# Kernel optimization log

Measured on AMD Instinct MI355X. Metric: run time of the kernel, lower is better.

The kernel has to match this reference:

```python
import jax, jax.numpy as jnp
import numpy as np
from jax import lax

_CLIP_MIN = 1e-06
_CLIP_MAX = 1.0
_POS_ALPHA = 0.0005
NUM_CLASSES = 21
RADIUS = 3
HALF_D = RADIUS * RADIUS
POOL = 3
PAD = POOL // 2
IGNORE = 255
LAM = 0.5  # loss_weight_lambda, lambda_way=1


def _max_pool(x):
    # NCHW max pool, kernel=stride=3, padding=1
    return lax.reduce_window(x, -jnp.inf, lax.max,
                             (1, 1, POOL, POOL), (1, 1, POOL, POOL),
                             ((0, 0), (0, 0), (PAD, PAD), (PAD, PAD)))


def _get_pairs(x):
    # stack radius*radius shifted crops -> [N, C, r^2, nh, nw]
    h, w = x.shape[2], x.shape[3]
    nh, nw = h - RADIUS + 1, w - RADIUS + 1
    crops = [x[:, :, y:y + nh, xo:xo + nw] for y in range(RADIUS) for xo in range(RADIUS)]
    return jnp.stack(crops, axis=2)


def _log_det_by_cholesky(m):
    chol = jnp.linalg.cholesky(m)
    return 2.0 * jnp.sum(jnp.log(jnp.diagonal(chol, axis1=-2, axis2=-1) + 1e-08), axis=-1)


def _rmi_lower_bound(labels_4d, probs_4d):
    la = _max_pool(labels_4d)
    pr = _max_pool(probs_4d)
    n, c = la.shape[0], la.shape[1]
    la_v = _get_pairs(la).reshape(n, c, HALF_D, -1)   # [N,C,d,L]
    pr_v = _get_pairs(pr).reshape(n, c, HALF_D, -1)
    la_v = la_v - jnp.mean(la_v, axis=3, keepdims=True)
    pr_v = pr_v - jnp.mean(pr_v, axis=3, keepdims=True)
    la_cov = jnp.einsum('ncdl,ncel->ncde', la_v, la_v)
    pr_cov = jnp.einsum('ncdl,ncel->ncde', pr_v, pr_v)
    eye = jnp.eye(HALF_D, dtype=la_cov.dtype)
    pr_cov_inv = jnp.linalg.inv(pr_cov + eye * _POS_ALPHA)
    la_pr_cov = jnp.einsum('ncdl,ncel->ncde', la_v, pr_v)
    appro_var = la_cov - jnp.einsum('ncde,ncef,ncgf->ncdg', la_pr_cov, pr_cov_inv, la_pr_cov)
    rmi_now = 0.5 * _log_det_by_cholesky(appro_var + eye * _POS_ALPHA)  # [N,C]
    rmi_per_class = jnp.mean(rmi_now.reshape(-1, NUM_CLASSES), axis=0) / float(HALF_D)
    return jnp.sum(rmi_per_class)


def setup_inputs() -> dict:
    key = jax.random.key(0)
    k1, k2 = jax.random.split(key)
    score = jax.random.normal(k1, (4, NUM_CLASSES, 512, 512), dtype=jnp.float32)
    target = jax.random.randint(k2, (4, 512, 512), 0, NUM_CLASSES, dtype=jnp.int64)
    return {"score": score, "target": target}


def reference(score, target):
    # cross entropy with ignore_index=255, mean reduction
    logp = jax.nn.log_softmax(score, axis=1)                      # [N,C,H,W]
    valid_ce = (target != IGNORE)
    safe_t = jnp.where(valid_ce, target, 0)
    nll = -jnp.take_along_axis(logp, safe_t[:, None].astype(jnp.int32), axis=1)[:, 0]
    normal_loss = jnp.sum(jnp.where(valid_ce, nll, 0.0)) / jnp.sum(valid_ce.astype(jnp.float32))

    # valid one-hot labels and masked sigmoid probs
    mask = (target < NUM_CLASSES)                                 # [N,H,W]
    maskf = mask.astype(jnp.float32)
    onehot = jax.nn.one_hot((target * mask).astype(jnp.int32), NUM_CLASSES, dtype=jnp.float32)
    onehot = onehot * maskf[..., None]                            # [N,H,W,C]
    onehot = jnp.transpose(onehot, (0, 3, 1, 2))                  # [N,C,H,W]
    probs = jnp.clip(jax.nn.sigmoid(score) * maskf[:, None], _CLIP_MIN, _CLIP_MAX)

    rmi_loss = _rmi_lower_bound(onehot, probs)
    return LAM * normal_loss + rmi_loss * (1.0 - LAM)
```

## Files before the change

kernel.cpp:

```cpp
#include <hip/hip_runtime.h>
#include <cfloat>
#include <cmath>

#define DEVINL __device__ __forceinline__

constexpr int N_ = 4, C_ = 21, H_ = 512, W_ = 512;
constexpr int P_ = 171;
constexpr int Q_ = 169;
constexpr int NC_ = N_ * C_;
constexpr int HW_ = H_ * W_;
constexpr int PP_ = P_ * P_;
constexpr int NCOV_ = 189;
constexpr float EPS_ = 5e-4f;
constexpr int RC_ = 29;
constexpr int G_ = 43;

DEVINL constexpr int tstart(int d) { return d * 9 - d * (d - 1) / 2; }

DEVINL float wave_sum(float v) {
#pragma unroll
    for (int o = 32; o > 0; o >>= 1) v += __shfl_down(v, o, 64);
    return v;
}

__global__ __launch_bounds__(256) void k_bits(const int* __restrict__ target,
                                              unsigned* __restrict__ pack) {
    int tid = blockIdx.x * 256 + threadIdx.x;
    if (tid >= N_ * PP_) return;
    int cell = tid % PP_;
    int n = tid / PP_;
    int j = cell % P_;
    int i = cell / P_;
    int hl = 3 * i - 1; if (hl < 0) hl = 0;
    int wl = 3 * j - 1; if (wl < 0) wl = 0;
    int hmax = 3 * i + 1, wmax = 3 * j + 1;
    const int* tb = target + (size_t)n * HW_;
    unsigned oh = 0, px = 0;
#pragma unroll
    for (int r = 0; r < 3; ++r) {
        int hh = hl + r;
        bool hv = hh <= hmax;
        const int* trow = tb + hh * W_;
#pragma unroll
        for (int dc = 0; dc < 3; ++dc) {
            int ww = wl + dc;
            int t = trow[ww];
            if (hv && (ww <= wmax) && t >= 0 && t < C_) {
                oh |= 1u << t;
                px |= 1u << (r * 3 + dc);
            }
        }
    }
    pack[tid] = oh | (px << 23);
}

__global__ __launch_bounds__(256) void k_ce(const float* __restrict__ score,
                                            const int* __restrict__ target,
                                            float* __restrict__ cov_ce) {
    int tid = blockIdx.x * 256 + threadIdx.x;
    int p0 = tid * 4;
    int n = p0 >> 18;
    int hw = p0 & (HW_ - 1);
    const float* sp = score + (size_t)n * C_ * HW_ + hw;

    float4 s[C_];
#pragma unroll
    for (int c = 0; c < C_; ++c)
        s[c] = *(const float4*)(sp + (size_t)c * HW_);
    int4 t4 = *(const int4*)(target + p0);

    float4 se = {0.f, 0.f, 0.f, 0.f};
    float4 stgt = {0.f, 0.f, 0.f, 0.f};
#pragma unroll
    for (int c = 0; c < C_; ++c) {
        se.x += __expf(s[c].x);
        se.y += __expf(s[c].y);
        se.z += __expf(s[c].z);
        se.w += __expf(s[c].w);
        if (t4.x == c) stgt.x = s[c].x;
        if (t4.y == c) stgt.y = s[c].y;
        if (t4.z == c) stgt.z = s[c].z;
        if (t4.w == c) stgt.w = s[c].w;
    }
    float nll = 0.f, cnt = 0.f;
    if (t4.x != 255) { nll += __logf(se.x) - stgt.x; cnt += 1.f; }
    if (t4.y != 255) { nll += __logf(se.y) - stgt.y; cnt += 1.f; }
    if (t4.z != 255) { nll += __logf(se.z) - stgt.z; cnt += 1.f; }
    if (t4.w != 255) { nll += __logf(se.w) - stgt.w; cnt += 1.f; }

    nll = wave_sum(nll);
    cnt = wave_sum(cnt);
    __shared__ float rn[4], rc[4];
    int wv = threadIdx.x >> 6, lane = threadIdx.x & 63;
    if (lane == 0) { rn[wv] = nll; rc[wv] = cnt; }
    __syncthreads();
    if (threadIdx.x == 0) {
        atomicAdd(&cov_ce[NC_ * NCOV_ + 0], rn[0] + rn[1] + rn[2] + rn[3]);
        atomicAdd(&cov_ce[NC_ * NCOV_ + 1], rc[0] + rc[1] + rc[2] + rc[3]);
    }
}

template <int IDX>
DEVINL void do_cell(const float (&f)[3][16], unsigned pk, int c, float* prp, float* lap) {
    unsigned px = pk >> 23;
    float vm = -FLT_MAX;
#pragma unroll
    for (int r = 0; r < 3; ++r)
#pragma unroll
        for (int dc = 0; dc < 3; ++dc)
            vm = fmaxf(vm, ((px >> (r * 3 + dc)) & 1u) ? f[r][IDX + dc] : -FLT_MAX);
    float p = __builtin_amdgcn_rcpf(1.f + __expf(-vm));
    p = fminf(fmaxf(p, 1e-6f), 1.f);
    *prp = p;
    *lap = ((pk >> c) & 1u) ? 1.f : 0.f;
}

__global__ __launch_bounds__(256) void k_pool(const float* __restrict__ score,
                                              const unsigned* __restrict__ pack,
                                              float* __restrict__ pr,
                                              float* __restrict__ la) {
    int tid = blockIdx.x * 256 + threadIdx.x;
    if (tid >= NC_ * P_ * G_) return;
    int g = tid % G_;
    int rest = tid / G_;
    int i = rest % P_;
    int ncidx = rest / P_;
    int n = ncidx / C_;
    int c = ncidx - n * C_;

    int hl = 3 * i - 1; if (hl < 0) hl = 0;
    int b = (g == 0) ? 0 : 12 * g - 4;
    int o3 = (b + 15 < W_) ? 12 : 8;

    const float* sb = score + (size_t)ncidx * HW_ + (size_t)hl * W_ + b;
    float f[3][16];
#pragma unroll
    for (int r = 0; r < 3; ++r) {
        const float* rp = sb + r * W_;
        float4 q0 = *(const float4*)(rp);
        float4 q1 = *(const float4*)(rp + 4);
        float4 q2 = *(const float4*)(rp + 8);
        float4 q3 = *(const float4*)(rp + o3);
        f[r][0] = q0.x;  f[r][1] = q0.y;  f[r][2] = q0.z;  f[r][3] = q0.w;
        f[r][4] = q1.x;  f[r][5] = q1.y;  f[r][6] = q1.z;  f[r][7] = q1.w;
        f[r][8] = q2.x;  f[r][9] = q2.y;  f[r][10] = q2.z; f[r][11] = q2.w;
        f[r][12] = q3.x; f[r][13] = q3.y; f[r][14] = q3.z; f[r][15] = q3.w;
    }

    const unsigned* pkp = pack + n * PP_ + i * P_ + 4 * g;
    size_t ob = (size_t)ncidx * PP_ + (size_t)i * P_ + 4 * g;
    if (g == 0) {
        do_cell<0>(f, pkp[0], c, pr + ob + 0, la + ob + 0);
        do_cell<2>(f, pkp[1], c, pr + ob + 1, la + ob + 1);
        do_cell<5>(f, pkp[2], c, pr + ob + 2, la + ob + 2);
        do_cell<8>(f, pkp[3], c, pr + ob + 3, la + ob + 3);
    } else {
        do_cell<3>(f, pkp[0], c, pr + ob + 0, la + ob + 0);
        do_cell<6>(f, pkp[1], c, pr + ob + 1, la + ob + 1);
        do_cell<9>(f, pkp[2], c, pr + ob + 2, la + ob + 2);
        if (4 * g + 3 < P_)
            do_cell<12>(f, pkp[3], c, pr + ob + 3, la + ob + 3);
    }
}

__global__ __launch_bounds__(256, 4) void k_cov(const float* __restrict__ la,
                                                const float* __restrict__ pr,
                                                float* __restrict__ cov) {
    int nc = blockIdx.x;
    int chunk = blockIdx.y;
    int part = blockIdx.z;
    int r0 = chunk * RC_;
    int rend = r0 + RC_;
    if (rend > Q_) rend = Q_;
    int npts = (rend - r0) * Q_;

    __shared__ float red[4][81];
    int lane = threadIdx.x & 63;
    int wv = threadIdx.x >> 6;

    if (part < 2) {
        const float* X = (part == 0 ? la : pr) + (size_t)nc * PP_;
        float s1[9], s2[45];
#pragma unroll
        for (int k = 0; k < 9; ++k) s1[k] = 0.f;
#pragma unroll
        for (int k = 0; k < 45; ++k) s2[k] = 0.f;
        for (int idx = threadIdx.x; idx < npts; idx += 256) {
            int lr = idx / Q_;
            int col = idx - lr * Q_;
            const float* xp = X + (r0 + lr) * P_ + col;
            float a[9];
#pragma unroll
            for (int dy = 0; dy < 3; ++dy)
#pragma unroll
                for (int dx = 0; dx < 3; ++dx) a[dy * 3 + dx] = xp[dy * P_ + dx];
#pragma unroll
            for (int d = 0; d < 9; ++d) s1[d] += a[d];
            int k = 0;
#pragma unroll
            for (int d = 0; d < 9; ++d)
#pragma unroll
                for (int e = d; e < 9; ++e) { s2[k] += a[d] * a[e]; ++k; }
        }
#pragma unroll
        for (int k = 0; k < 9; ++k) { float v = wave_sum(s1[k]); if (lane == 0) red[wv][k] = v; }
#pragma unroll
        for (int k = 0; k < 45; ++k) { float v = wave_sum(s2[k]); if (lane == 0) red[wv][9 + k] = v; }
        __syncthreads();
        int b1 = (part == 0) ? 0 : 9;
        int b2 = (part == 0) ? 18 : 63;
        for (int k = threadIdx.x; k < 54; k += 256) {
            float v = red[0][k] + red[1][k] + red[2][k] + red[3][k];
            int dst = (k < 9) ? (b1 + k) : (b2 + k - 9);
            atomicAdd(&cov[nc * NCOV_ + dst], v);
        }
    } else {
        const float* A = la + (size_t)nc * PP_;
        const float* B = pr + (size_t)nc * PP_;
        float sab[81];
#pragma unroll
        for (int k = 0; k < 81; ++k) sab[k] = 0.f;
        for (int idx = threadIdx.x; idx < npts; idx += 256) {
            int lr = idx / Q_;
            int col = idx - lr * Q_;
            const float* ap = A + (r0 + lr) * P_ + col;
            const float* bp = B + (r0 + lr) * P_ + col;
            float a[9], b[9];
#pragma unroll
            for (int dy = 0; dy < 3; ++dy)
#pragma unroll
                for (int dx = 0; dx < 3; ++dx) {
                    a[dy * 3 + dx] = ap[dy * P_ + dx];
                    b[dy * 3 + dx] = bp[dy * P_ + dx];
                }
#pragma unroll
            for (int d = 0; d < 9; ++d)
#pragma unroll
                for (int e = 0; e < 9; ++e) sab[d * 9 + e] += a[d] * b[e];
        }
#pragma unroll
        for (int k = 0; k < 81; ++k) { float v = wave_sum(sab[k]); if (lane == 0) red[wv][k] = v; }
        __syncthreads();
        for (int k = threadIdx.x; k < 81; k += 256) {
            float v = red[0][k] + red[1][k] + red[2][k] + red[3][k];
            atomicAdd(&cov[nc * NCOV_ + 108 + k], v);
        }
    }
}

__global__ __launch_bounds__(128) void k_final(const float* __restrict__ cov,
                                               float* __restrict__ out) {
    __shared__ float red[128];
    int t = threadIdx.x;
    float my = 0.f;
    if (t < NC_) {
        const float* S = cov + t * NCOV_;
        const float Lf = (float)(Q_ * Q_);
        float sA[9], sB[9];
#pragma unroll
        for (int d = 0; d < 9; ++d) { sA[d] = S[d]; sB[d] = S[9 + d]; }
        float laC[45], M[45], Cm[81];
        {
            int k = 0;
#pragma unroll
            for (int d = 0; d < 9; ++d)
#pragma unroll
                for (int e = d; e < 9; ++e) {
                    laC[k] = S[18 + k] - sA[d] * sA[e] / Lf;
                    M[k] = S[63 + k] - sB[d] * sB[e] / Lf + (d == e ? EPS_ : 0.f);
                    ++k;
                }
#pragma unroll
            for (int d = 0; d < 9; ++d)
#pragma unroll
                for (int e = 0; e < 9; ++e)
                    Cm[d * 9 + e] = S[108 + d * 9 + e] - sA[d] * sB[e] / Lf;
        }
#pragma unroll
        for (int j = 0; j < 9; ++j) {
            float s = M[tstart(j)];
#pragma unroll
            for (int k = 0; k < j; ++k) { float l = M[tstart(k) + (j - k)]; s -= l * l; }
            float dj = sqrtf(fmaxf(s, 1e-30f));
            M[tstart(j)] = dj;
            float inv = 1.f / dj;
#pragma unroll
            for (int i = j + 1; i < 9; ++i) {
                float s2 = M[tstart(j) + (i - j)];
#pragma unroll
                for (int k = 0; k < j; ++k)
                    s2 -= M[tstart(k) + (i - k)] * M[tstart(k) + (j - k)];
                M[tstart(j) + (i - j)] = s2 * inv;
            }
        }
#pragma unroll
        for (int p = 0; p < 9; ++p) {
#pragma unroll
            for (int i = 0; i < 9; ++i) {
                float s = Cm[p * 9 + i];
#pragma unroll
                for (int k = 0; k < i; ++k)
                    s -= M[tstart(k) + (i - k)] * Cm[p * 9 + k];
                Cm[p * 9 + i] = s / M[tstart(i)];
            }
        }
#pragma unroll
        for (int d = 0; d < 9; ++d)
#pragma unroll
            for (int e = d; e < 9; ++e) {
                float s = 0.f;
#pragma unroll
                for (int i = 0; i < 9; ++i) s += Cm[d * 9 + i] * Cm[e * 9 + i];
                laC[tstart(d) + (e - d)] -= s;
                if (d == e) laC[tstart(d)] += EPS_;
            }
        float rmi = 0.f;
#pragma unroll
        for (int j = 0; j < 9; ++j) {
            float s = laC[tstart(j)];
#pragma unroll
            for (int k = 0; k < j; ++k) { float l = laC[tstart(k) + (j - k)]; s -= l * l; }
            float dj = sqrtf(fmaxf(s, 0.f));
            laC[tstart(j)] = dj;
            float inv = 1.f / fmaxf(dj, 1e-30f);
#pragma unroll
            for (int i = j + 1; i < 9; ++i) {
                float s2 = laC[tstart(j) + (i - j)];
#pragma unroll
                for (int k = 0; k < j; ++k)
                    s2 -= laC[tstart(k) + (i - k)] * laC[tstart(k) + (j - k)];
                laC[tstart(j) + (i - j)] = s2 * inv;
            }
            rmi += __logf(dj + 1e-8f);
        }
        my = rmi;
    }
    red[t] = my;
    __syncthreads();
#pragma unroll
    for (int o = 64; o > 0; o >>= 1) {
        if (t < o) red[t] += red[t + o];
        __syncthreads();
    }
    if (t == 0) {
        float rmi_total = red[0] / 36.f;
        float ce = cov[NC_ * NCOV_ + 0] / cov[NC_ * NCOV_ + 1];
        out[0] = 0.5f * ce + 0.5f * rmi_total;
    }
}

extern "C" void kernel_launch(void* const* d_in, const int* in_sizes, int n_in,
                              void* d_out, int out_size, void* d_ws, size_t ws_size,
                              hipStream_t stream) {
    const float* score = (const float*)d_in[0];
    const int* target = (const int*)d_in[1];
    float* pr = (float*)d_ws;
    float* la = pr + (size_t)NC_ * PP_;
    float* cov = la + (size_t)NC_ * PP_;
    unsigned* pack = (unsigned*)(cov + NC_ * NCOV_ + 2);
    hipMemsetAsync(cov, 0, (size_t)(NC_ * NCOV_ + 2) * sizeof(float), stream);

    k_bits<<<dim3((N_ * PP_ + 255) / 256), dim3(256), 0, stream>>>(target, pack);
    k_ce<<<dim3(N_ * HW_ / 4 / 256), dim3(256), 0, stream>>>(score, target, cov);
    k_pool<<<dim3((NC_ * P_ * G_ + 255) / 256), dim3(256), 0, stream>>>(score, pack, pr, la);
    k_cov<<<dim3(NC_, 6, 3), dim3(256), 0, stream>>>(la, pr, cov);
    k_final<<<dim3(1), dim3(128), 0, stream>>>(cov, (float*)d_out);
}
```

Measured before the change: 254.4 us.

## Pad pooled rows to 172 and vectorize covariance loads over 4-column strips

Pooled label/prob maps are now stored with a 172-float row pitch so each row is 16-byte aligned. The covariance kernel then has each thread handle four adjacent output columns, loading a 3x8 window with float4 reads instead of nine scalar loads per point. This reuses overlapping window values across neighbouring points and cuts load instruction count. Register pressure rises, especially in the cross-covariance branch, which now holds 48 window values plus 81 accumulators, and the occupancy hint was dropped from the launch bounds. The last 8-wide read in each row runs into the row padding, whose values are never written and are only used by masked-off columns.

```diff
diff --git a/kernel.cpp b/kernel.cpp
--- a/kernel.cpp
+++ b/kernel.cpp
@@ -10,6 +10,8 @@
 constexpr int NC_ = N_ * C_;
 constexpr int HW_ = H_ * W_;
 constexpr int PP_ = P_ * P_;
+constexpr int PROW_ = 172;
+constexpr int PPAD_ = PROW_ * P_;
 constexpr int NCOV_ = 189;
 constexpr float EPS_ = 5e-4f;
 constexpr int RC_ = 29;
@@ -148,7 +150,7 @@
     }
 
     const unsigned* pkp = pack + n * PP_ + i * P_ + 4 * g;
-    size_t ob = (size_t)ncidx * PP_ + (size_t)i * P_ + 4 * g;
+    size_t ob = (size_t)ncidx * PPAD_ + (size_t)i * PROW_ + 4 * g;
     if (g == 0) {
         do_cell<0>(f, pkp[0], c, pr + ob + 0, la + ob + 0);
         do_cell<2>(f, pkp[1], c, pr + ob + 1, la + ob + 1);
@@ -163,87 +165,109 @@
     }
 }
 
-__global__ __launch_bounds__(256, 4) void k_cov(const float* __restrict__ la,
-                                                const float* __restrict__ pr,
-                                                float* __restrict__ cov) {
+__global__ __launch_bounds__(256) void k_cov(const float* __restrict__ la,
+                                             const float* __restrict__ pr,
+                                             float* __restrict__ cov) {
     int nc = blockIdx.x;
     int chunk = blockIdx.y;
     int part = blockIdx.z;
     int r0 = chunk * RC_;
     int rend = r0 + RC_;
     if (rend > Q_) rend = Q_;
-    int npts = (rend - r0) * Q_;
+    int nitems = (rend - r0) * G_;
 
     __shared__ float red[4][81];
     int lane = threadIdx.x & 63;
     int wv = threadIdx.x >> 6;
 
     if (part < 2) {
-        const float* X = (part == 0 ? la : pr) + (size_t)nc * PP_;
+        const float* X = (part == 0 ? la : pr) + (size_t)nc * PPAD_;
         float s1[9], s2[45];
 #pragma unroll
         for (int k = 0; k < 9; ++k) s1[k] = 0.f;
 #pragma unroll
         for (int k = 0; k < 45; ++k) s2[k] = 0.f;
-        for (int idx = threadIdx.x; idx < npts; idx += 256) {
-            int lr = idx / Q_;
-            int col = idx - lr * Q_;
-            const float* xp = X + (r0 + lr) * P_ + col;
-            float a[9];
-#pragma unroll
-            for (int dy = 0; dy < 3; ++dy)
-#pragma unroll
-                for (int dx = 0; dx < 3; ++dx) a[dy * 3 + dx] = xp[dy * P_ + dx];
-#pragma unroll
-            for (int d = 0; d < 9; ++d) s1[d] += a[d];
-            int k = 0;
-#pragma unroll
-            for (int d = 0; d < 9; ++d)
-#pragma unroll
-                for (int e = d; e < 9; ++e) { s2[k] += a[d] * a[e]; ++k; }
-        }
-#pragma unroll
-        for (int k = 0; k < 9; ++k) { float v = wave_sum(s1[k]); if (lane == 0) red[wv][k] = v; }
-#pragma unroll
-        for (int k = 0; k < 45; ++k) { float v = wave_sum(s2[k]); if (lane == 0) red[wv][9 + k] = v; }
+        for (int idx = threadIdx.x; idx < nitems; idx += 256) {
+            int lr = idx / G_;
+            int q = idx - lr * G_;
+            int x0 = q * 4;
+            const float* base = X + (r0 + lr) * PROW_ + x0;
+            float v[3][8];
+#pragma unroll
+            for (int r = 0; r < 3; ++r) {
+                float4 u0 = *(const float4*)(base + r * PROW_);
+                float4 u1 = *(const float4*)(base + r * PROW_ + 4);
+                v[r][0] = u0.x; v[r][1] = u0.y; v[r][2] = u0.z; v[r][3] = u0.w;
+                v[r][4] = u1.x; v[r][5] = u1.y; v[r][6] = u1.z; v[r][7] = u1.w;
+            }
+#pragma unroll
+            for (int p = 0; p < 4; ++p) {
+                if (x0 + p < Q_) {
+#pragma unroll
+                    for (int d = 0; d < 9; ++d) s1[d] += v[d / 3][p + d % 3];
+                    int k = 0;
+#pragma unroll
+                    for (int d = 0; d < 9; ++d)
+#pragma unroll
+                        for (int e = d; e < 9; ++e) {
+                            s2[k] += v[d / 3][p + d % 3] * v[e / 3][p + e % 3];
+                            ++k;
+                        }
+                }
+            }
+        }
+#pragma unroll
+        for (int k = 0; k < 9; ++k) { float v2 = wave_sum(s1[k]); if (lane == 0) red[wv][k] = v2; }
+#pragma unroll
+        for (int k = 0; k < 45; ++k) { float v2 = wave_sum(s2[k]); if (lane == 0) red[wv][9 + k] = v2; }
         __syncthreads();
         int b1 = (part == 0) ? 0 : 9;
         int b2 = (part == 0) ? 18 : 63;
         for (int k = threadIdx.x; k < 54; k += 256) {
-            float v = red[0][k] + red[1][k] + red[2][k] + red[3][k];
+            float v2 = red[0][k] + red[1][k] + red[2][k] + red[3][k];
             int dst = (k < 9) ? (b1 + k) : (b2 + k - 9);
-            atomicAdd(&cov[nc * NCOV_ + dst], v);
+            atomicAdd(&cov[nc * NCOV_ + dst], v2);
         }
     } else {
-        const float* A = la + (size_t)nc * PP_;
-        const float* B = pr + (size_t)nc * PP_;
+        const float* A = la + (size_t)nc * PPAD_;
+        const float* B = pr + (size_t)nc * PPAD_;
         float sab[81];
 #pragma unroll
         for (int k = 0; k < 81; ++k) sab[k] = 0.f;
-        for (int idx = threadIdx.x; idx < npts; idx += 256) {
-            int lr = idx / Q_;
-            int col = idx - lr * Q_;
-            const float* ap = A + (r0 + lr) * P_ + col;
-            const float* bp = B + (r0 + lr) * P_ + col;
-            float a[9], b[9];
-#pragma unroll
-            for (int dy = 0; dy < 3; ++dy)
-#pragma unroll
-                for (int dx = 0; dx < 3; ++dx) {
-                    a[dy * 3 + dx] = ap[dy * P_ + dx];
-                    b[dy * 3 + dx] = bp[dy * P_ + dx];
+        for (int idx = threadIdx.x; idx < nitems; idx += 256) {
+            int lr = idx / G_;
+            int q = idx - lr * G_;
+            int x0 = q * 4;
+            size_t off = (size_t)(r0 + lr) * PROW_ + x0;
+            float a[3][8], b[3][8];
+#pragma unroll
+            for (int r = 0; r < 3; ++r) {
+                float4 u0 = *(const float4*)(A + off + r * PROW_);
+                float4 u1 = *(const float4*)(A + off + r * PROW_ + 4);
+                a[r][0] = u0.x; a[r][1] = u0.y; a[r][2] = u0.z; a[r][3] = u0.w;
+                a[r][4] = u1.x; a[r][5] = u1.y; a[r][6] = u1.z; a[r][7] = u1.w;
+                float4 w0 = *(const float4*)(B + off + r * PROW_);
+                float4 w1 = *(const float4*)(B + off + r * PROW_ + 4);
+                b[r][0] = w0.x; b[r][1] = w0.y; b[r][2] = w0.z; b[r][3] = w0.w;
+                b[r][4] = w1.x; b[r][5] = w1.y; b[r][6] = w1.z; b[r][7] = w1.w;
+            }
+#pragma unroll
+            for (int p = 0; p < 4; ++p) {
+                if (x0 + p < Q_) {
+#pragma unroll
+                    for (int d = 0; d < 9; ++d)
+#pragma unroll
+                        for (int e = 0; e < 9; ++e)
+                            sab[d * 9 + e] += a[d / 3][p + d % 3] * b[e / 3][p + e % 3];
                 }
-#pragma unroll
-            for (int d = 0; d < 9; ++d)
-#pragma unroll
-                for (int e = 0; e < 9; ++e) sab[d * 9 + e] += a[d] * b[e];
-        }
-#pragma unroll
-        for (int k = 0; k < 81; ++k) { float v = wave_sum(sab[k]); if (lane == 0) red[wv][k] = v; }
+            }
+        }
+#pragma unroll
+        for (int k = 0; k < 81; ++k) { float v2 = wave_sum(sab[k]); if (lane == 0) red[wv][k] = v2; }
         __syncthreads();
         for (int k = threadIdx.x; k < 81; k += 256) {
-            float v = red[0][k] + red[1][k] + red[2][k] + red[3][k];
-            atomicAdd(&cov[nc * NCOV_ + 108 + k], v);
+            float v2 = red[0][k] + red[1][k] + red[2][k] + red[3][k];
+            atomicAdd(&cov[nc * NCOV_ + 108 + k], v2);
         }
     }
 }
@@ -355,8 +379,8 @@
     const float* score = (const float*)d_in[0];
     const int* target = (const int*)d_in[1];
     float* pr = (float*)d_ws;
-    float* la = pr + (size_t)NC_ * PP_;
-    float* cov = la + (size_t)NC_ * PP_;
+    float* la = pr + (size_t)NC_ * PPAD_;
+    float* cov = la + (size_t)NC_ * PPAD_;
     unsigned* pack = (unsigned*)(cov + NC_ * NCOV_ + 2);
     hipMemsetAsync(cov, 0, (size_t)(NC_ * NCOV_ + 2) * sizeof(float), stream);
 
```

Result: no change. 254.1 us (-0.1%).
